# Performance work log

Hardware: AMD Instinct MI355X
Metric: run time of the kernel (lower is better)

## Reference

```python
import jax, jax.numpy as jnp
import numpy as np

N = 100000; E = 1600000
X_DIM = 128; Y_DIM = 32; H_DIM = 128; R_DIM = 128; Z_DIM = 64
TAU = 1.0; KEEP = 0.1  # dropout p=0.9 -> keep prob 0.1


def spmm(edge_index, edge_weight, h):
    # out[row] += w * h[col]  (sparse [N,N] @ dense [N,D])
    row, col = edge_index[0], edge_index[1]
    return jax.ops.segment_sum(h[col] * edge_weight[:, None], row, num_segments=N)


def setup_inputs() -> dict:
    key = jax.random.key(0)
    ks = jax.random.split(key, 32)
    p = lambda k, shp: (0.02 * jax.random.normal(k, shp)).astype(jnp.float32)
    inp = {
        'x': jax.random.normal(ks[0], (N, X_DIM), dtype=jnp.float32),
        'y_': jax.random.uniform(ks[1], (N, Y_DIM), dtype=jnp.float32),
        'edge_index': jax.random.randint(ks[2], (2, E), 0, N, dtype=jnp.int32),
        'edge_weight': jax.random.uniform(ks[3], (E,), dtype=jnp.float32),
        'non_label': jax.random.bernoulli(ks[4], 0.5, (N,)),
        # inverted dropout mask, torch semantics: keep w.p. 0.1, scale by 1/0.1
        'dropout_mask': (jax.random.bernoulli(ks[5], KEEP, (N, X_DIM)).astype(jnp.float32) / KEEP),
        'u_gumbel': jax.random.uniform(ks[6], (N, Y_DIM), dtype=jnp.float32),
        'z_eps': jax.random.normal(ks[7], (Z_DIM,), dtype=jnp.float32),
        # x_to_yu (2-layer spmm GCN)
        'Wg1': p(ks[8], (X_DIM, H_DIM)), 'bg1': jnp.zeros((H_DIM,), jnp.float32),
        'Wg2': p(ks[9], (H_DIM, Y_DIM)), 'bg2': jnp.zeros((Y_DIM,), jnp.float32),
        # GSNN_Encoder
        'W_xy': p(ks[10], (H_DIM + Y_DIM, R_DIM)), 'b_xy': jnp.zeros((R_DIM,), jnp.float32),
        'W_hr': p(ks[11], (R_DIM, R_DIM)), 'b_hr': jnp.zeros((R_DIM,), jnp.float32),
        # R_to_MuSigma
        'W_rh': p(ks[12], (R_DIM, R_DIM)), 'b_rh': jnp.zeros((R_DIM,), jnp.float32),
        'W_mu': p(ks[13], (R_DIM, Z_DIM)), 'b_mu': jnp.zeros((Z_DIM,), jnp.float32),
        'W_sig': p(ks[14], (R_DIM, Z_DIM)), 'b_sig': jnp.zeros((Z_DIM,), jnp.float32),
        # GSNN_Decoder
        'W_xh': p(ks[15], (X_DIM, H_DIM)), 'b_xh': jnp.zeros((H_DIM,), jnp.float32),
        'W_h2': p(ks[16], (H_DIM + Z_DIM, H_DIM + Z_DIM)), 'b_h2': jnp.zeros((H_DIM + Z_DIM,), jnp.float32),
        'W_hy': p(ks[17], (H_DIM + Z_DIM, Y_DIM)), 'b_hy': jnp.zeros((Y_DIM,), jnp.float32),
    }
    return inp


def reference(x, y_, edge_index, edge_weight, non_label, dropout_mask, u_gumbel, z_eps,
              Wg1, bg1, Wg2, bg2, W_xy, b_xy, W_hr, b_hr,
              W_rh, b_rh, W_mu, b_mu, W_sig, b_sig,
              W_xh, b_xh, W_h2, b_h2, W_hy, b_hy):
    # ---- x_to_yu: 2-layer spmm GCN -> (y_encode [N,Y], y_embedding [N,H]) ----
    h_emb = jax.nn.relu(spmm(edge_index, edge_weight, x) @ Wg1 + bg1)
    y_encode = spmm(edge_index, edge_weight, h_emb) @ Wg2 + bg2
    # ---- gumbel_softmax(hard=True, tau=1) at non-labelled nodes ----
    g = -jnp.log(-jnp.log(u_gumbel + 1e-10) + 1e-10)
    soft = jax.nn.softmax((y_encode + g) / TAU, axis=-1)
    hard = jax.nn.one_hot(jnp.argmax(soft, axis=-1), Y_DIM, dtype=soft.dtype)
    y_gumbel = hard + soft - jax.lax.stop_gradient(soft)  # straight-through
    y = jnp.where(non_label[:, None], y_gumbel, y_)
    # ---- GSNN_Encoder (adj unused, matching original) ----
    h_enc = jax.nn.relu(jnp.concatenate([h_emb, y], axis=1) @ W_xy + b_xy)
    r_nodes = h_enc @ W_hr + b_hr
    r_graph = jnp.mean(r_nodes, axis=0)  # readout [R]
    # ---- R_to_MuSigma + rsample ----
    hr = jax.nn.relu(r_graph @ W_rh + b_rh)
    mu = hr @ W_mu + b_mu
    sigma = 0.1 + 0.9 * jax.nn.sigmoid(hr @ W_sig + b_sig)
    z = mu + sigma * z_eps  # Normal.rsample
    # ---- GSNN_Decoder ----
    xd = x * dropout_mask
    h = jax.nn.relu(xd @ W_xh + b_xh)
    h = jnp.concatenate([h, jnp.broadcast_to(z, (h.shape[0], Z_DIM))], axis=1)
    h = h / (jnp.linalg.norm(h, axis=1, keepdims=True) + 1e-06)
    h = jax.nn.relu(spmm(edge_index, edge_weight, h) @ W_h2 + b_h2)
    y_pred = spmm(edge_index, edge_weight, h) @ W_hy + b_hy
    return y_pred
```

## Files before the change

kernel.cpp:

```cpp
#include <hip/hip_runtime.h>
#include <hip/hip_bf16.h>

#define NN 100000
#define EE 1600000

typedef unsigned short u16;
typedef unsigned int   u32;
typedef short short8 __attribute__((ext_vector_type(8)));
typedef float v4f    __attribute__((ext_vector_type(4)));
typedef u32 u32x2    __attribute__((ext_vector_type(2)));

__device__ __forceinline__ float b2f(u16 h){ u32 u = ((u32)h) << 16; return __builtin_bit_cast(float, u); }
__device__ __forceinline__ float lo2f(u32 u){ return __builtin_bit_cast(float, u << 16); }
__device__ __forceinline__ float hi2f(u32 u){ return __builtin_bit_cast(float, u & 0xffff0000u); }
__device__ __forceinline__ u16   f2b(float f){ __hip_bfloat16 h = __float2bfloat16(f); return __builtin_bit_cast(u16, h); }
__device__ __forceinline__ float ldx(const void* p, long i, int fm){
  return fm ? ((const float*)p)[i] : b2f(((const u16*)p)[i]);
}
__device__ __forceinline__ float i2f(int v){ return __builtin_bit_cast(float, v); }

__global__ void k_detect(const void* __restrict__ x, const void* __restrict__ nonlab,
                         int* __restrict__ flags){
  __shared__ int s_bad, s_ni, s_nf, s_nb;
  int t = threadIdx.x;
  if (t == 0){ s_bad = 0; s_ni = 0; s_nf = 0; s_nb = 0; }
  __syncthreads();
  u32 w = ((const u32*)x)[t];
  u32 lo = w & 0xffffu, ex = (lo >> 7) & 0xffu;
  if (lo != 0u && (ex < 100u || ex > 140u)) atomicAdd(&s_bad, 1);
  if (t < 64){
    u32 v = ((const u32*)nonlab)[t];
    if (v > 1u) atomicAdd(&s_ni, 1);
    if (v != 0u && v != 0x3F800000u) atomicAdd(&s_nf, 1);
  }
  if (t < 128){
    u16 h = ((const u16*)nonlab)[t];
    if (h != 0 && h != 0x3F80) atomicAdd(&s_nb, 1);
  }
  __syncthreads();
  if (t == 0){
    flags[0] = (s_bad > 32) ? 1 : 0;
    flags[1] = (s_ni == 0) ? 1 : ((s_nf == 0) ? 3 : ((s_nb == 0) ? 2 : 0));
  }
}

#define PW_G1 0
#define PW_G2 16384
#define PW_XY 20480
#define PW_XH 40960
#define PW_H2 57344
#define PW_HY 94208
#define PW_TOT 100352
#define PB_G1 0
#define PB_XY 128
#define PB_XH 256
#define PB_H2 384
#define PB_ZERO 576
#define PB_HY 704
#define PB_TOT 736

__global__ __launch_bounds__(256) void k_pack(const void* W0, const void* W1, const void* W2,
                      const void* W3, const void* W4, const void* W5,
                      const void* b0, const void* b1, const void* b2, const void* b3, const void* b4,
                      u16* __restrict__ Wp, float* __restrict__ bp, const int* __restrict__ flags){
  int e = blockIdx.x * 256 + threadIdx.x;
  int fm = flags[0];
  if (e < PW_TOT){
    const void* src; int off, DOUT;
    if      (e < PW_G2){ src = W0; off = PW_G1; DOUT = 128; }
    else if (e < PW_XY){ src = W1; off = PW_G2; DOUT = 32; }
    else if (e < PW_XH){ src = W2; off = PW_XY; DOUT = 128; }
    else if (e < PW_H2){ src = W3; off = PW_XH; DOUT = 128; }
    else if (e < PW_HY){ src = W4; off = PW_H2; DOUT = 192; }
    else               { src = W5; off = PW_HY; DOUT = 32; }
    int local = e - off;
    int k = local / DOUT, col = local - k * DOUT;
    u16 v = fm ? f2b(((const float*)src)[local]) : ((const u16*)src)[local];
    Wp[off + ((k >> 3) * DOUT + col) * 8 + (k & 7)] = v;
  }
  int eb = e - PW_TOT;
  if (eb >= 0 && eb < PB_TOT){
    float v = 0.f;
    if      (eb < 128) v = ldx(b0, eb, fm);
    else if (eb < 256) v = ldx(b1, eb - 128, fm);
    else if (eb < 384) v = ldx(b2, eb - 256, fm);
    else if (eb < 576) v = ldx(b3, eb - 384, fm);
    else if (eb < 704) v = 0.f;
    else               v = ldx(b4, eb - 704, fm);
    bp[eb] = v;
  }
}

#define BSH 9
#define NBK 196
#define CAP 16384

__global__ __launch_bounds__(256) void k_binA(const int* __restrict__ ei, const void* __restrict__ ew,
                      int* __restrict__ bcnt, int2* __restrict__ stage,
                      const int* __restrict__ flags){
  __shared__ int lcnt[NBK];
  __shared__ int lbase[NBK];
  int t = threadIdx.x;
  for (int i = t; i < NBK; i += 256) lcnt[i] = 0;
  __syncthreads();
  int fm = flags[0];
  long e0 = (long)blockIdx.x * 4096;
  int bb[16], ord[16], pk[16], wb[16];
  #pragma unroll
  for (int j = 0; j < 16; ++j){
    long e = e0 + j * 256 + t;
    bool v = e < EE;
    int r = v ? ei[e] : 0;
    int c = v ? ei[EE + e] : 0;
    float w = v ? ldx(ew, e, fm) : 0.f;
    int b = r >> BSH;
    bb[j] = v ? b : -1;
    pk[j] = ((r & 511) << 17) | c;
    wb[j] = __builtin_bit_cast(int, w);
    if (v) ord[j] = atomicAdd(&lcnt[b], 1);
  }
  __syncthreads();
  for (int i = t; i < NBK; i += 256){
    int c = lcnt[i];
    lbase[i] = c ? atomicAdd(&bcnt[i], c) : 0;
  }
  __syncthreads();
  #pragma unroll
  for (int j = 0; j < 16; ++j){
    if (bb[j] >= 0){
      int pos = lbase[bb[j]] + ord[j];
      if (pos < CAP) stage[(long)bb[j] * CAP + pos] = make_int2(pk[j], wb[j]);
    }
  }
}

__global__ void k_scanB(const int* __restrict__ bcnt, int* __restrict__ bbase,
                        int* __restrict__ rowptr){
  __shared__ int l[256];
  int t = threadIdx.x;
  int v = (t < NBK) ? bcnt[t] : 0;
  l[t] = v; __syncthreads();
  for (int o = 1; o < 256; o <<= 1){
    int x = (t >= o) ? l[t - o] : 0; __syncthreads();
    l[t] += x; __syncthreads();
  }
  if (t < NBK) bbase[t] = l[t] - v;
  if (t == 0) rowptr[NN] = EE;
}

__global__ __launch_bounds__(512) void k_binB(const int* __restrict__ bbase, const int* __restrict__ bcnt,
                      const int2* __restrict__ stage, int2* __restrict__ cpk,
                      int* __restrict__ rowptr){
  __shared__ int cnt[512];
  __shared__ int cur[512];
  int b = blockIdx.x, t = threadIdx.x;
  int r0 = b << BSH;
  int rows = min(512, NN - r0);
  cnt[t] = 0; __syncthreads();
  int cb = min(bcnt[b], CAP);
  const int2* sb = stage + (long)b * CAP;
  for (int j = t; j < cb; j += 512)
    atomicAdd(&cnt[((u32)sb[j].x) >> 17], 1);
  __syncthreads();
  int v = cnt[t];
  cur[t] = v; __syncthreads();
  for (int o = 1; o < 512; o <<= 1){
    int x = (t >= o) ? cur[t - o] : 0; __syncthreads();
    cur[t] += x; __syncthreads();
  }
  int excl = bbase[b] + cur[t] - v;
  if (t < rows) rowptr[r0 + t] = excl;
  __syncthreads();
  cur[t] = excl;
  __syncthreads();
  for (int j = t; j < cb; j += 512){
    int2 w = sb[j];
    int rib = ((u32)w.x) >> 17;
    int pos = atomicAdd(&cur[rib], 1);
    cpk[pos] = make_int2(w.x & 0x1FFFF, w.y);
  }
}

template<bool AG, bool EPI>
__global__ __launch_bounds__(256) void k_spmm(const u16* __restrict__ in, u16* __restrict__ out,
                       const int* __restrict__ rowptr, const int2* __restrict__ cpk,
                       const float* __restrict__ agt, float* __restrict__ agg,
                       const float* __restrict__ bias){
  int wid  = blockIdx.x * 4 + (threadIdx.x >> 6);
  int lane = threadIdx.x & 63;
  if (wid >= NN) return;
  int half = lane >> 5, l16 = lane & 31;
  int s = rowptr[wid], e = rowptr[wid + 1];
  float a0 = 0.f, a1 = 0.f, a2 = 0.f, a3 = 0.f, aga = 0.f;
  for (int j = s; j < e; j += 8){
    int2 pe[4];
    if (j + 8 <= e){
      #pragma unroll
      for (int k = 0; k < 4; ++k) pe[k] = cpk[j + 2 * k + half];
    } else {
      #pragma unroll
      for (int k = 0; k < 4; ++k){
        int idx = j + 2 * k + half;
        int2 w = cpk[idx < e ? idx : j];
        if (idx >= e) w.y = 0;
        pe[k] = w;
      }
    }
    u32x2 u[4];
    #pragma unroll
    for (int k = 0; k < 4; ++k)
      u[k] = *(const u32x2*)(in + (long)pe[k].x * 128 + 4 * l16);
    if (AG && l16 == 0){
      #pragma unroll
      for (int k = 0; k < 4; ++k) aga = fmaf(i2f(pe[k].y), agt[pe[k].x], aga);
    }
    #pragma unroll
    for (int k = 0; k < 4; ++k){
      float wt = i2f(pe[k].y);
      a0 = fmaf(wt, lo2f(u[k].x), a0);
      a1 = fmaf(wt, hi2f(u[k].x), a1);
      a2 = fmaf(wt, lo2f(u[k].y), a2);
      a3 = fmaf(wt, hi2f(u[k].y), a3);
    }
  }
  a0 += __shfl_xor(a0, 32); a1 += __shfl_xor(a1, 32);
  a2 += __shfl_xor(a2, 32); a3 += __shfl_xor(a3, 32);
  if (AG) aga += __shfl_xor(aga, 32);
  if (EPI){
    a0 = fmaxf(a0 + bias[4 * l16],     0.f);
    a1 = fmaxf(a1 + bias[4 * l16 + 1], 0.f);
    a2 = fmaxf(a2 + bias[4 * l16 + 2], 0.f);
    a3 = fmaxf(a3 + bias[4 * l16 + 3], 0.f);
  }
  if (half == 0){
    u32x2 w;
    w.x = (u32)f2b(a0) | ((u32)f2b(a1) << 16);
    w.y = (u32)f2b(a2) | ((u32)f2b(a3) << 16);
    *(u32x2*)(out + (long)wid * 128 + 4 * l16) = w;
    if (AG && l16 == 0) agg[wid] = aga;
  }
}

__global__ __launch_bounds__(256) void k_spmm32b(const u16* __restrict__ in, void* __restrict__ out,
                       const int* __restrict__ rowptr, const int2* __restrict__ cpk,
                       const int* __restrict__ flags, const float* __restrict__ bp){
  int row = blockIdx.x * 16 + (threadIdx.x >> 4);
  int d = threadIdx.x & 15;
  if (row >= NN) return;
  int fm = flags[0];
  int s = rowptr[row], e = rowptr[row + 1];
  float a0 = bp[2 * d], a1 = bp[2 * d + 1];
  for (int j = s; j < e; j += 8){
    int2 p[8];
    if (j + 8 <= e){
      #pragma unroll
      for (int q = 0; q < 8; ++q) p[q] = cpk[j + q];
    } else {
      #pragma unroll
      for (int q = 0; q < 8; ++q){
        int idx = j + q;
        int2 w = cpk[idx < e ? idx : j];
        if (idx >= e) w.y = 0;
        p[q] = w;
      }
    }
    u32 u[8];
    #pragma unroll
    for (int q = 0; q < 8; ++q) u[q] = *(const u32*)(in + (long)p[q].x * 32 + 2 * d);
    #pragma unroll
    for (int q = 0; q < 8; ++q){
      float wt = i2f(p[q].y);
      a0 = fmaf(wt, lo2f(u[q]), a0); a1 = fmaf(wt, hi2f(u[q]), a1);
    }
  }
  if (fm){
    *(float2*)((float*)out + (long)row * 32 + 2 * d) = make_float2(a0, a1);
  } else {
    u32 w = (u32)f2b(a0) | ((u32)f2b(a1) << 16);
    *(u32*)((u16*)out + (long)row * 32 + 2 * d) = w;
  }
}

__global__ __launch_bounds__(256) void k_spmmg(const u16* __restrict__ in, u16* __restrict__ y,
                       const int* __restrict__ rowptr, const int2* __restrict__ cpk,
                       const int* __restrict__ flags, const void* __restrict__ bg2,
                       const void* __restrict__ ug, const void* __restrict__ ylab,
                       const void* __restrict__ nonlab){
  int row = blockIdx.x * 16 + (threadIdx.x >> 4);
  int d = threadIdx.x & 15;
  if (row >= NN) return;
  int fm = flags[0], mode = flags[1];
  bool nl;
  if      (mode == 1) nl = ((const int*)nonlab)[row] != 0;
  else if (mode == 3) nl = ((const float*)nonlab)[row] != 0.f;
  else if (mode == 2) nl = ((const u16*)nonlab)[row] != 0;
  else                nl = ((const unsigned char*)nonlab)[row] != 0;
  long base = (long)row * 32;
  if (!nl){
    u32 lo, hi;
    if (fm){
      lo = (u32)f2b(((const float*)ylab)[base + 2 * d]);
      hi = (u32)f2b(((const float*)ylab)[base + 2 * d + 1]);
    } else {
      lo = ((const u16*)ylab)[base + 2 * d];
      hi = ((const u16*)ylab)[base + 2 * d + 1];
    }
    *(u32*)(y + base + 2 * d) = lo | (hi << 16);
    return;
  }
  int s = rowptr[row], e = rowptr[row + 1];
  float a0 = 0.f, a1 = 0.f;
  for (int j = s; j < e; j += 8){
    int2 p[8];
    if (j + 8 <= e){
      #pragma unroll
      for (int q = 0; q < 8; ++q) p[q] = cpk[j + q];
    } else {
      #pragma unroll
      for (int q = 0; q < 8; ++q){
        int idx = j + q;
        int2 w = cpk[idx < e ? idx : j];
        if (idx >= e) w.y = 0;
        p[q] = w;
      }
    }
    u32 u[8];
    #pragma unroll
    for (int q = 0; q < 8; ++q) u[q] = *(const u32*)(in + (long)p[q].x * 32 + 2 * d);
    #pragma unroll
    for (int q = 0; q < 8; ++q){
      float wt = i2f(p[q].y);
      a0 = fmaf(wt, lo2f(u[q]), a0); a1 = fmaf(wt, hi2f(u[q]), a1);
    }
  }
  float u0 = ldx(ug, base + 2 * d,     fm);
  float u1 = ldx(ug, base + 2 * d + 1, fm);
  float g0 = -logf(-logf(u0 + 1e-10f) + 1e-10f);
  float g1 = -logf(-logf(u1 + 1e-10f) + 1e-10f);
  float v0 = a0 + ldx(bg2, 2 * d,     fm) + g0;
  float v1 = a1 + ldx(bg2, 2 * d + 1, fm) + g1;
  float bm; int bi;
  if (v0 >= v1){ bm = v0; bi = 2 * d; } else { bm = v1; bi = 2 * d + 1; }
  #pragma unroll
  for (int o = 1; o < 16; o <<= 1){
    float om = __shfl_xor(bm, o);
    int   oi = __shfl_xor(bi, o);
    if (om > bm || (om == bm && oi < bi)){ bm = om; bi = oi; }
  }
  u32 lo = (2 * d     == bi) ? 0x3F80u : 0u;
  u32 hi = (2 * d + 1 == bi) ? 0x3F80u : 0u;
  *(u32*)(y + base + 2 * d) = lo | (hi << 16);
}

template<int K, int DOUT, int CT, int RTW, bool RELU, int AMODE, int OMODE, bool CSUM>
__global__ __launch_bounds__(256) void k_mm(const u16* __restrict__ A, const void* __restrict__ A2,
     const void* __restrict__ A3, const u16* __restrict__ Wp, const float* __restrict__ bp,
     void* __restrict__ outv, const int* __restrict__ flags, float* __restrict__ csacc){
  constexpr int STEPS = K / 32;
  constexpr int G = DOUT / (16 * CT);
  constexpr int CHUNKS = 6250 / RTW;
  __shared__ float lsum[128];
  int wid = blockIdx.x * 4 + (threadIdx.x >> 6);
  if (wid >= G * CHUNKS) return;
  int g = wid % G; long chunk = wid / G;
  int lane = threadIdx.x & 63, n = lane & 15, q = lane >> 4;
  int colOff = g * CT * 16;
  int fm = (AMODE == 4) ? flags[0] : 0;

  if (CSUM){
    if (threadIdx.x < 128) lsum[threadIdx.x] = 0.f;
    __syncthreads();
  }

  short8 B[CT][STEPS];
  float bv[CT];
  #pragma unroll
  for (int ct = 0; ct < CT; ++ct){
    int col = colOff + ct * 16 + n;
    bv[ct] = bp[col];
    #pragma unroll
    for (int s = 0; s < STEPS; ++s)
      B[ct][s] = *(const short8*)(Wp + (((s * 4 + q) * DOUT) + col) * 8);
  }

  float csum[CT];
  #pragma unroll
  for (int ct = 0; ct < CT; ++ct) csum[ct] = 0.f;

  for (int rt = 0; rt < RTW; ++rt){
    long rowbase = (chunk * RTW + rt) * 16;
    long arow = rowbase + n;
    float agr = (AMODE == 3) ? ((const float*)A2)[arow] : 0.f;
    v4f acc[CT] = {};
    #pragma unroll
    for (int s = 0; s < STEPS; ++s){
      short8 a;
      if (AMODE == 0){
        a = *(const short8*)(A + arow * K + s * 32 + q * 8);
      } else if (AMODE == 2){
        if (s < 4) a = *(const short8*)(A + arow * 128 + s * 32 + q * 8);
        else       a = *(const short8*)((const u16*)A2 + arow * 32 + q * 8);
      } else if (AMODE == 3){
        if (s < 4) a = *(const short8*)(A + arow * 128 + s * 32 + q * 8);
        else {
          const float* zv = (const float*)A3;
          #pragma unroll
          for (int j = 0; j < 8; ++j) a[j] = (short)f2b(agr * zv[(s - 4) * 32 + q * 8 + j]);
        }
      } else {
        long base = arow * 128 + s * 32 + q * 8;
        if (fm){
          const float* xp = (const float*)A2 + base;
          float4 x0 = *(const float4*)xp, x1 = *(const float4*)(xp + 4);
          a[0] = (short)f2b(x0.x); a[1] = (short)f2b(x0.y);
          a[2] = (short)f2b(x0.z); a[3] = (short)f2b(x0.w);
          a[4] = (short)f2b(x1.x); a[5] = (short)f2b(x1.y);
          a[6] = (short)f2b(x1.z); a[7] = (short)f2b(x1.w);
        } else {
          a = *(const short8*)((const u16*)A2 + base);
        }
      }
      #pragma unroll
      for (int ct = 0; ct < CT; ++ct)
        acc[ct] = __builtin_amdgcn_mfma_f32_16x16x32_bf16(a, B[ct][s], acc[ct], 0, 0, 0);
    }
    long orow = rowbase + q * 4;
    #pragma unroll
    for (int ct = 0; ct < CT; ++ct){
      int col = colOff + ct * 16 + n;
      #pragma unroll
      for (int r = 0; r < 4; ++r){
        float v = acc[ct][r] + bv[ct];
        if (RELU) v = fmaxf(v, 0.f);
        if (CSUM) csum[ct] += v;
        if (OMODE != 3){
          long oi = (orow + r) * (long)DOUT + col;
          if (OMODE == 2) ((float*)outv)[oi] = v;
          else            ((u16*)outv)[oi] = f2b(v);
        }
      }
    }
  }
  if (CSUM){
    #pragma unroll
    for (int ct = 0; ct < CT; ++ct){
      csum[ct] += __shfl_xor(csum[ct], 16);
      csum[ct] += __shfl_xor(csum[ct], 32);
      if (lane < 16) atomicAdd(&lsum[colOff + ct * 16 + n], csum[ct]);
    }
    __syncthreads();
    if (threadIdx.x < 128) csacc[(long)blockIdx.x * 128 + threadIdx.x] = lsum[threadIdx.x];
  }
}

__global__ __launch_bounds__(256) void k_csred(const float* __restrict__ pb, float* __restrict__ accum){
  __shared__ float l[256];
  int c = blockIdx.x, t = threadIdx.x;
  float s = 0.f;
  for (int r = t; r < 1563; r += 256) s += pb[(long)r * 128 + c];
  l[t] = s; __syncthreads();
  for (int o = 128; o; o >>= 1){ if (t < o) l[t] += l[t + o]; __syncthreads(); }
  if (t == 0) accum[c] = l[0];
}

__global__ __launch_bounds__(256) void k_mmnorm(const void* __restrict__ A2, const void* __restrict__ A3,
     const u16* __restrict__ Wp, const float* __restrict__ bp,
     u16* __restrict__ outHs, float* __restrict__ ag,
     const float* __restrict__ zbuf, const int* __restrict__ flags){
  constexpr int STEPS = 4, CT = 8, CHUNKS = 6250;
  int wid = blockIdx.x * 4 + (threadIdx.x >> 6);
  if (wid >= CHUNKS) return;
  long chunk = wid;
  int lane = threadIdx.x & 63, n = lane & 15, q = lane >> 4;
  int fm = flags[0];

  short8 B[CT][STEPS];
  float bv[CT];
  #pragma unroll
  for (int ct = 0; ct < CT; ++ct){
    int col = ct * 16 + n;
    bv[ct] = bp[col];
    #pragma unroll
    for (int s = 0; s < STEPS; ++s)
      B[ct][s] = *(const short8*)(Wp + (((s * 4 + q) * 128) + col) * 8);
  }
  float zz = zbuf[64];

  {
    long rowbase = chunk * 16;
    long arow = rowbase + n;
    v4f acc[CT] = {};
    #pragma unroll
    for (int s = 0; s < STEPS; ++s){
      short8 a;
      long base = arow * 128 + s * 32 + q * 8;
      if (fm){
        const float* xp = (const float*)A2 + base;
        const float* dp = (const float*)A3 + base;
        float4 x0 = *(const float4*)xp, x1 = *(const float4*)(xp + 4);
        float4 d0 = *(const float4*)dp, d1 = *(const float4*)(dp + 4);
        a[0] = (short)f2b(x0.x * d0.x); a[1] = (short)f2b(x0.y * d0.y);
        a[2] = (short)f2b(x0.z * d0.z); a[3] = (short)f2b(x0.w * d0.w);
        a[4] = (short)f2b(x1.x * d1.x); a[5] = (short)f2b(x1.y * d1.y);
        a[6] = (short)f2b(x1.z * d1.z); a[7] = (short)f2b(x1.w * d1.w);
      } else {
        short8 xv = *(const short8*)((const u16*)A2 + base);
        short8 dv = *(const short8*)((const u16*)A3 + base);
        #pragma unroll
        for (int j = 0; j < 8; ++j) a[j] = (short)f2b(b2f((u16)xv[j]) * b2f((u16)dv[j]));
      }
      #pragma unroll
      for (int ct = 0; ct < CT; ++ct)
        acc[ct] = __builtin_amdgcn_mfma_f32_16x16x32_bf16(a, B[ct][s], acc[ct], 0, 0, 0);
    }
    float v[CT][4];
    float sqr[4] = {0.f, 0.f, 0.f, 0.f};
    #pragma unroll
    for (int ct = 0; ct < CT; ++ct){
      #pragma unroll
      for (int r = 0; r < 4; ++r){
        float t = fmaxf(acc[ct][r] + bv[ct], 0.f);
        v[ct][r] = t;
        sqr[r] += t * t;
      }
    }
    #pragma unroll
    for (int r = 0; r < 4; ++r){
      #pragma unroll
      for (int o = 1; o < 16; o <<= 1) sqr[r] += __shfl_xor(sqr[r], o);
    }
    float scale[4];
    #pragma unroll
    for (int r = 0; r < 4; ++r) scale[r] = 1.f / (sqrtf(sqr[r] + zz) + 1e-6f);
    long orow = rowbase + q * 4;
    #pragma unroll
    for (int ct = 0; ct < CT; ++ct){
      int col = ct * 16 + n;
      #pragma unroll
      for (int r = 0; r < 4; ++r)
        outHs[(orow + r) * 128 + col] = f2b(v[ct][r] * scale[r]);
    }
    if (n == 0){
      #pragma unroll
      for (int r = 0; r < 4; ++r) ag[orow + r] = scale[r];
    }
  }
}

__global__ void k_z(const float* __restrict__ accum,
                    const void* Whr, const void* bhr, const void* Wrh, const void* brh,
                    const void* Wmu, const void* bmu, const void* Wsig, const void* bsig,
                    const void* zeps, float* __restrict__ zout, const int* __restrict__ flags){
  __shared__ float hm[128], rg[128], hr[128], zl[64];
  int t = threadIdx.x, fm = flags[0];
  hm[t] = accum[t] * (1.0f / 100000.0f);
  __syncthreads();
  { float s = ldx(bhr, t, fm);
    for (int k = 0; k < 128; ++k) s = fmaf(hm[k], ldx(Whr, (long)k * 128 + t, fm), s);
    rg[t] = s; }
  __syncthreads();
  { float s = ldx(brh, t, fm);
    for (int k = 0; k < 128; ++k) s = fmaf(rg[k], ldx(Wrh, (long)k * 128 + t, fm), s);
    hr[t] = fmaxf(s, 0.f); }
  __syncthreads();
  if (t < 64){
    float m = ldx(bmu, t, fm), sv = ldx(bsig, t, fm);
    for (int k = 0; k < 128; ++k){
      float h = hr[k];
      m  = fmaf(h, ldx(Wmu,  (long)k * 64 + t, fm), m);
      sv = fmaf(h, ldx(Wsig, (long)k * 64 + t, fm), sv);
    }
    float sig = 0.1f + 0.9f / (1.f + expf(-sv));
    float z = fmaf(sig, ldx(zeps, t, fm), m);
    zl[t] = z; zout[t] = z;
  }
  __syncthreads();
  if (t == 0){ float ss = 0.f; for (int j = 0; j < 64; ++j) ss += zl[j] * zl[j]; zout[64] = ss; }
}

extern "C" void kernel_launch(void* const* d_in, const int* in_sizes, int n_in,
                              void* d_out, int out_size, void* d_ws, size_t ws_size,
                              hipStream_t stream){
  const void* x    = d_in[0];
  const void* ylab = d_in[1];
  const int*  ei   = (const int*)d_in[2];
  const void* ew   = d_in[3];
  const void* nonlab = d_in[4];
  const void* dm   = d_in[5];
  const void* ug   = d_in[6];
  const void* zeps = d_in[7];
  const void* Wg1 = d_in[8],  *bg1 = d_in[9];
  const void* Wg2 = d_in[10], *bg2 = d_in[11];
  const void* Wxy = d_in[12], *bxy = d_in[13];
  const void* Whr = d_in[14], *bhr = d_in[15];
  const void* Wrh = d_in[16], *brh = d_in[17];
  const void* Wmu = d_in[18], *bmu = d_in[19];
  const void* Wsg = d_in[20], *bsg = d_in[21];
  const void* Wxh = d_in[22], *bxh = d_in[23];
  const void* Wh2 = d_in[24], *bh2 = d_in[25];
  const void* Why = d_in[26], *bhy = d_in[27];

  char* ws = (char*)d_ws;
  size_t off = 0;
  auto alloc = [&](size_t bytes){ void* p = ws + off; off += (bytes + 511) & ~(size_t)511; return p; };
  int*   flags  = (int*)  alloc(256);
  int*   rowptr = (int*)  alloc((size_t)(NN + 1) * 4);
  int*   bbase  = (int*)  alloc(1024 * 4);
  float* accum  = (float*)alloc(1024 * 4);
  u16*   Wpack  = (u16*)  alloc((size_t)PW_TOT * 2);
  float* bpack  = (float*)alloc((size_t)PB_TOT * 4);
  float* AG1    = (float*)alloc((size_t)NN * 4);
  float* AG2    = (float*)alloc((size_t)NN * 4);
  float* pb     = (float*)alloc((size_t)1563 * 128 * 4);
  int2*  cpk    = (int2*) alloc((size_t)EE * 8);
  u16*   B0     = (u16*)  alloc((size_t)NN * 192 * 2);
  u16*   B1     = (u16*)  alloc((size_t)NN * 192 * 2);
  u16* yproj = B0 + (size_t)NN * 128;
  u16* ybuf  = B1 + (size_t)NN * 160;
  int2* stage = (int2*)B0;
  u16* tbuf = B0;
  int* bcnt = (int*)(accum + 512);

  hipMemsetAsync(accum, 0, 1024 * 4, stream);
  k_detect<<<1, 256, 0, stream>>>(x, nonlab, flags);
  k_pack<<<(PW_TOT + PB_TOT + 255) / 256, 256, 0, stream>>>(Wg1, Wg2, Wxy, Wxh, Wh2, Why,
                                                            bg1, bxy, bxh, bh2, bhy, Wpack, bpack, flags);
  k_binA <<<(EE + 4095) / 4096, 256, 0, stream>>>(ei, ew, bcnt, stage, flags);
  k_scanB<<<1, 256, 0, stream>>>(bcnt, bbase, rowptr);
  k_binB <<<NBK, 512, 0, stream>>>(bbase, bcnt, stage, cpk, rowptr);
  k_mm<128,128,4,2,false,4,0,false><<<1563, 256, 0, stream>>>(nullptr, x, nullptr, Wpack + PW_G1, bpack + PB_ZERO, B1, flags, nullptr);
  k_spmm<false,true ><<<25000, 256, 0, stream>>>(B1, B0, rowptr, cpk, nullptr, nullptr, bpack + PB_G1);
  k_mm<128,32 ,2,1,false,0,0,false><<<1563, 256, 0, stream>>>(B0, nullptr, nullptr, Wpack + PW_G2, bpack + PB_ZERO, yproj, flags, nullptr);
  k_spmmg<<<6250, 256, 0, stream>>>(yproj, ybuf, rowptr, cpk, flags, bg2, ug, ylab, nonlab);
  k_mm<160,128,4,2,true ,2,3,true ><<<1563, 256, 0, stream>>>(B0, ybuf, nullptr, Wpack + PW_XY, bpack + PB_XY, nullptr, flags, pb);
  k_csred<<<128, 256, 0, stream>>>(pb, accum);
  k_z<<<1, 128, 0, stream>>>(accum, Whr, bhr, Wrh, brh, Wmu, bmu, Wsg, bsg, zeps, accum + 128, flags);
  k_mmnorm<<<1563, 256, 0, stream>>>(x, dm, Wpack + PW_XH, bpack + PB_XH, B1, AG1, accum + 128, flags);
  k_spmm<true ,false><<<25000, 256, 0, stream>>>(B1, B0, rowptr, cpk, AG1, AG2, nullptr);
  k_mm<192,192,4,2,true ,3,0,false><<<2344, 256, 0, stream>>>(B0, AG2, accum + 128, Wpack + PW_H2, bpack + PB_H2, B1, flags, nullptr);
  k_mm<192,32 ,2,1,false,0,0,false><<<1563, 256, 0, stream>>>(B1, nullptr, nullptr, Wpack + PW_HY, bpack + PB_ZERO, tbuf, flags, nullptr);
  k_spmm32b<<<6250, 256, 0, stream>>>(tbuf, d_out, rowptr, cpk, flags, bpack + PB_HY);
}
```

Baseline: 588.6 us.

## Fuse H2 and HY matmuls via LDS staging; split spmm32b edges across half-groups

Replaces the two separate GEMM launches (192x192 with ReLU, then 192x32) with one kernel. Each block computes a 32-row tile of the hidden layer, stages it in shared memory as bf16, and has wave 0 apply W_hy directly, so the 100000x192 intermediate never goes to global memory. The final spmm kernel now has two half-groups of 8 lanes handle alternating edges with 8-byte loads, then combines them with a shuffle. In exchange, only one of four waves does the second matmul, and the fused kernel adds barriers.

```diff
diff --git a/kernel.cpp b/kernel.cpp
--- a/kernel.cpp
+++ b/kernel.cpp
@@ -247,37 +247,49 @@
   int row = blockIdx.x * 16 + (threadIdx.x >> 4);
   int d = threadIdx.x & 15;
   if (row >= NN) return;
+  int eh = d >> 3, d8 = d & 7;
   int fm = flags[0];
   int s = rowptr[row], e = rowptr[row + 1];
-  float a0 = bp[2 * d], a1 = bp[2 * d + 1];
+  float a0 = 0.f, a1 = 0.f, a2 = 0.f, a3 = 0.f;
   for (int j = s; j < e; j += 8){
-    int2 p[8];
+    int2 p[4];
     if (j + 8 <= e){
       #pragma unroll
-      for (int q = 0; q < 8; ++q) p[q] = cpk[j + q];
+      for (int k = 0; k < 4; ++k) p[k] = cpk[j + 2 * k + eh];
     } else {
       #pragma unroll
-      for (int q = 0; q < 8; ++q){
-        int idx = j + q;
+      for (int k = 0; k < 4; ++k){
+        int idx = j + 2 * k + eh;
         int2 w = cpk[idx < e ? idx : j];
         if (idx >= e) w.y = 0;
-        p[q] = w;
-      }
-    }
-    u32 u[8];
-    #pragma unroll
-    for (int q = 0; q < 8; ++q) u[q] = *(const u32*)(in + (long)p[q].x * 32 + 2 * d);
-    #pragma unroll
-    for (int q = 0; q < 8; ++q){
-      float wt = i2f(p[q].y);
-      a0 = fmaf(wt, lo2f(u[q]), a0); a1 = fmaf(wt, hi2f(u[q]), a1);
-    }
-  }
-  if (fm){
-    *(float2*)((float*)out + (long)row * 32 + 2 * d) = make_float2(a0, a1);
-  } else {
-    u32 w = (u32)f2b(a0) | ((u32)f2b(a1) << 16);
-    *(u32*)((u16*)out + (long)row * 32 + 2 * d) = w;
+        p[k] = w;
+      }
+    }
+    u32x2 u[4];
+    #pragma unroll
+    for (int k = 0; k < 4; ++k) u[k] = *(const u32x2*)(in + (long)p[k].x * 32 + 4 * d8);
+    #pragma unroll
+    for (int k = 0; k < 4; ++k){
+      float wt = i2f(p[k].y);
+      a0 = fmaf(wt, lo2f(u[k].x), a0);
+      a1 = fmaf(wt, hi2f(u[k].x), a1);
+      a2 = fmaf(wt, lo2f(u[k].y), a2);
+      a3 = fmaf(wt, hi2f(u[k].y), a3);
+    }
+  }
+  a0 += __shfl_xor(a0, 8); a1 += __shfl_xor(a1, 8);
+  a2 += __shfl_xor(a2, 8); a3 += __shfl_xor(a3, 8);
+  a0 += bp[4 * d8]; a1 += bp[4 * d8 + 1]; a2 += bp[4 * d8 + 2]; a3 += bp[4 * d8 + 3];
+  if (eh == 0){
+    if (fm){
+      float4 w = make_float4(a0, a1, a2, a3);
+      *(float4*)((float*)out + (long)row * 32 + 4 * d8) = w;
+    } else {
+      u32x2 w;
+      w.x = (u32)f2b(a0) | ((u32)f2b(a1) << 16);
+      w.y = (u32)f2b(a2) | ((u32)f2b(a3) << 16);
+      *(u32x2*)((u16*)out + (long)row * 32 + 4 * d8) = w;
+    }
   }
 }
 
@@ -390,7 +402,6 @@
   for (int rt = 0; rt < RTW; ++rt){
     long rowbase = (chunk * RTW + rt) * 16;
     long arow = rowbase + n;
-    float agr = (AMODE == 3) ? ((const float*)A2)[arow] : 0.f;
     v4f acc[CT] = {};
     #pragma unroll
     for (int s = 0; s < STEPS; ++s){
@@ -400,13 +411,6 @@
       } else if (AMODE == 2){
         if (s < 4) a = *(const short8*)(A + arow * 128 + s * 32 + q * 8);
         else       a = *(const short8*)((const u16*)A2 + arow * 32 + q * 8);
-      } else if (AMODE == 3){
-        if (s < 4) a = *(const short8*)(A + arow * 128 + s * 32 + q * 8);
-        else {
-          const float* zv = (const float*)A3;
-          #pragma unroll
-          for (int j = 0; j < 8; ++j) a[j] = (short)f2b(agr * zv[(s - 4) * 32 + q * 8 + j]);
-        }
       } else {
         long base = arow * 128 + s * 32 + q * 8;
         if (fm){
@@ -450,6 +454,81 @@
     }
     __syncthreads();
     if (threadIdx.x < 128) csacc[(long)blockIdx.x * 128 + threadIdx.x] = lsum[threadIdx.x];
+  }
+}
+
+__global__ __launch_bounds__(256) void k_mmh2(const u16* __restrict__ A, const float* __restrict__ AG2,
+     const float* __restrict__ zbuf, const u16* __restrict__ Wh2p, const float* __restrict__ bh2p,
+     const u16* __restrict__ Whyp, u16* __restrict__ tbuf){
+  __shared__ u16 hl[16][200];
+  int w = threadIdx.x >> 6;
+  int lane = threadIdx.x & 63, n = lane & 15, q = lane >> 4;
+  int colOff = w * 48;
+
+  short8 B[3][6];
+  float bv[3];
+  #pragma unroll
+  for (int ct = 0; ct < 3; ++ct){
+    int col = colOff + ct * 16 + n;
+    bv[ct] = bh2p[col];
+    #pragma unroll
+    for (int s = 0; s < 6; ++s)
+      B[ct][s] = *(const short8*)(Wh2p + (((s * 4 + q) * 192) + col) * 8);
+  }
+  short8 B2[2][6];
+  if (w == 0){
+    #pragma unroll
+    for (int ct = 0; ct < 2; ++ct){
+      int col = ct * 16 + n;
+      #pragma unroll
+      for (int s = 0; s < 6; ++s)
+        B2[ct][s] = *(const short8*)(Whyp + (((s * 4 + q) * 32) + col) * 8);
+    }
+  }
+
+  for (int rt = 0; rt < 2; ++rt){
+    long rowbase = ((long)blockIdx.x * 2 + rt) * 16;
+    long arow = rowbase + n;
+    float agr = AG2[arow];
+    v4f acc[3] = {};
+    #pragma unroll
+    for (int s = 0; s < 6; ++s){
+      short8 a;
+      if (s < 4) a = *(const short8*)(A + arow * 128 + s * 32 + q * 8);
+      else {
+        #pragma unroll
+        for (int j = 0; j < 8; ++j) a[j] = (short)f2b(agr * zbuf[(s - 4) * 32 + q * 8 + j]);
+      }
+      #pragma unroll
+      for (int ct = 0; ct < 3; ++ct)
+        acc[ct] = __builtin_amdgcn_mfma_f32_16x16x32_bf16(a, B[ct][s], acc[ct], 0, 0, 0);
+    }
+    #pragma unroll
+    for (int ct = 0; ct < 3; ++ct){
+      int col = colOff + ct * 16 + n;
+      #pragma unroll
+      for (int r = 0; r < 4; ++r)
+        hl[q * 4 + r][col] = f2b(fmaxf(acc[ct][r] + bv[ct], 0.f));
+    }
+    __syncthreads();
+    if (w == 0){
+      v4f a2[2] = {};
+      #pragma unroll
+      for (int s = 0; s < 6; ++s){
+        short8 a = *(const short8*)(&hl[n][s * 32 + q * 8]);
+        #pragma unroll
+        for (int ct = 0; ct < 2; ++ct)
+          a2[ct] = __builtin_amdgcn_mfma_f32_16x16x32_bf16(a, B2[ct][s], a2[ct], 0, 0, 0);
+      }
+      #pragma unroll
+      for (int ct = 0; ct < 2; ++ct){
+        int col = ct * 16 + n;
+        #pragma unroll
+        for (int r = 0; r < 4; ++r)
+          tbuf[(rowbase + q * 4 + r) * 32 + col] = f2b(a2[ct][r]);
+      }
+    }
+    __syncthreads();
   }
 }
 
@@ -618,7 +697,7 @@
   u16* yproj = B0 + (size_t)NN * 128;
   u16* ybuf  = B1 + (size_t)NN * 160;
   int2* stage = (int2*)B0;
-  u16* tbuf = B0;
+  u16* tbuf = B1;
   int* bcnt = (int*)(accum + 512);
 
   hipMemsetAsync(accum, 0, 1024 * 4, stream);
@@ -637,7 +716,7 @@
   k_z<<<1, 128, 0, stream>>>(accum, Whr, bhr, Wrh, brh, Wmu, bmu, Wsg, bsg, zeps, accum + 128, flags);
   k_mmnorm<<<1563, 256, 0, stream>>>(x, dm, Wpack + PW_XH, bpack + PB_XH, B1, AG1, accum + 128, flags);
   k_spmm<true ,false><<<25000, 256, 0, stream>>>(B1, B0, rowptr, cpk, AG1, AG2, nullptr);
-  k_mm<192,192,4,2,true ,3,0,false><<<2344, 256, 0, stream>>>(B0, AG2, accum + 128, Wpack + PW_H2, bpack + PB_H2, B1, flags, nullptr);
-  k_mm<192,32 ,2,1,false,0,0,false><<<1563, 256, 0, stream>>>(B1, nullptr, nullptr, Wpack + PW_HY, bpack + PB_ZERO, tbuf, flags, nullptr);
+  k_mmh2<<<3125, 256, 0, stream>>>(B0, AG2, accum + 128, Wpack + PW_H2, bpack + PB_H2,
+                                   Wpack + PW_HY, tbuf);
   k_spmm32b<<<6250, 256, 0, stream>>>(tbuf, d_out, rowptr, cpk, flags, bpack + PB_HY);
 }
```

Measured after the change: 580.5 us. No clear change (-1.4%).
